# Kernel optimization log

Measured on AMD Instinct MI355X. Metric: run time of the kernel, lower is better.

## Reference

```python
import jax, jax.numpy as jnp
import numpy as np

N_NODES = 50000
N_EDGES = 800000
HIDDEN = 64


def _init_linear(key, fan_in, fan_out):
    kw, kb = jax.random.split(key)
    lim = 1.0 / np.sqrt(fan_in)
    W = jax.random.uniform(kw, (fan_in, fan_out), jnp.float32, -lim, lim)
    b = jax.random.uniform(kb, (fan_out,), jnp.float32, -lim, lim)
    return W, b


def setup_inputs() -> dict:
    key = jax.random.key(0)
    ks = jax.random.split(key, 10)
    feat = jax.random.normal(ks[0], (N_NODES, HIDDEN), jnp.float32)
    x = jax.random.normal(ks[1], (N_NODES, 3), jnp.float32)
    src = jax.random.randint(ks[2], (N_EDGES,), 0, N_NODES, jnp.int32)
    dst = jax.random.randint(ks[3], (N_EDGES,), 0, N_NODES, jnp.int32)
    # message MLP: (2H+1) -> H -> H, relu after both layers (last_activation=mid)
    W1, b1 = _init_linear(ks[4], 2 * HIDDEN + 1, HIDDEN)
    W2, b2 = _init_linear(ks[5], HIDDEN, HIDDEN)
    # soft edge gate: H -> 1
    we, be = _init_linear(ks[6], HIDDEN, 1)
    # update MLP: H -> H -> H, relu mid, no last activation
    U1, c1 = _init_linear(ks[7], HIDDEN, HIDDEN)
    U2, c2 = _init_linear(ks[8], HIDDEN, HIDDEN)
    return dict(feat=feat, x=x, src=src, dst=dst,
                W1=W1, b1=b1, W2=W2, b2=b2, we=we, be=be,
                U1=U1, c1=c1, U2=U2, c2=c2)


def reference(feat, x, src, dst, W1, b1, W2, b2, we, be, U1, c1, U2, c2):
    # per-edge squared distance between endpoint coordinates: [E, 1]
    sqd = jnp.sum((x[src] - x[dst]) ** 2, axis=-1, keepdims=True)
    # message input: [E, 2H+1]
    msg_in = jnp.concatenate([feat[src], feat[dst], sqd], axis=-1)
    # 2-layer message MLP with relu mid and last activation
    m = jax.nn.relu(jax.nn.relu(msg_in @ W1 + b1) @ W2 + b2)
    # sigmoid soft-edge gate: [E, 1]
    gate = jax.nn.sigmoid(m @ we + be)
    # scatter-sum gated messages to destination nodes: [N, H]
    m_sum = jax.ops.segment_sum(m * gate, dst, num_segments=N_NODES)
    # node update MLP on (m_sum + feat), residual add
    h = m_sum + feat
    h_new = jax.nn.relu(h @ U1 + c1) @ U2 + c2
    return h_new + feat
```

## Files before the change

kernel.cpp:

```cpp
#include <hip/hip_runtime.h>
#include <hip/hip_bf16.h>
#include <stdint.h>

#define N_NODES 50000
#define N_EDGES 800000
#define HDIM 64
#define SCAN_N (N_NODES + 1)

#define MSG_BYTES  ((size_t)N_EDGES * HDIM * 2)
#define INT_OFF    MSG_BYTES
#define DEG_OFF    (INT_OFF)
#define OFFS_OFF   (INT_OFF + 204800)
#define POS_OFF    (INT_OFF + 409600)
#define FB_OFF     (INT_OFF + 614400)
#define W1T_OFF    (FB_OFF + (size_t)N_NODES * HDIM * 2)
#define W2T_OFF    (W1T_OFF + 16384)
#define U1T_OFF    (W2T_OFF + 8192)
#define U2T_OFF    (U1T_OFF + 8192)
#define WS_NEED    (U2T_OFF + 8192)

typedef __attribute__((ext_vector_type(8))) short short8;
typedef __attribute__((ext_vector_type(4))) float floatx4;

__device__ __forceinline__ float bf2f(unsigned short u) {
    union { unsigned int i; float f; } v; v.i = ((unsigned int)u) << 16; return v.f;
}
__device__ __forceinline__ unsigned short f2bf(float f) {
    __hip_bfloat16 h = __float2bfloat16(f);
    return *reinterpret_cast<unsigned short*>(&h);
}

__device__ __forceinline__ int detect_is_bf16(const unsigned short* p) {
    int cnt = 0;
    #pragma unroll
    for (int i = 0; i < 64; ++i) {
        unsigned short b = p[i];
        int e = (b >> 7) & 0xFF;
        cnt += ((e >= 97 && e <= 157) || (b & 0x7FFF) == 0) ? 1 : 0;
    }
    return cnt >= 56;
}

__device__ __forceinline__ float getf(const void* p, unsigned int i, int isb) {
    return isb ? bf2f(((const unsigned short*)p)[i]) : ((const float*)p)[i];
}

__device__ __forceinline__ short8 get8bf(const void* p, unsigned int i, int isb) {
    if (isb) {
        return *reinterpret_cast<const short8*>((const short*)p + i);
    } else {
        const float4 f0 = *reinterpret_cast<const float4*>((const float*)p + i);
        const float4 f1 = *reinterpret_cast<const float4*>((const float*)p + i + 4);
        short8 a;
        a[0] = (short)f2bf(f0.x); a[1] = (short)f2bf(f0.y);
        a[2] = (short)f2bf(f0.z); a[3] = (short)f2bf(f0.w);
        a[4] = (short)f2bf(f1.x); a[5] = (short)f2bf(f1.y);
        a[6] = (short)f2bf(f1.z); a[7] = (short)f2bf(f1.w);
        return a;
    }
}

#define COMPILER_FENCE() asm volatile("" ::: "memory")
#define WAIT_LDS() __builtin_amdgcn_s_waitcnt(0xC07F)

__global__ __launch_bounds__(256) void cvt_kernel(const void* __restrict__ feat,
                                                  unsigned short* __restrict__ fb) {
    const int isb = detect_is_bf16((const unsigned short*)feat);
    int i = (blockIdx.x * 256 + threadIdx.x) * 8;
    if (i >= N_NODES * HDIM) return;
    if (isb) {
        *reinterpret_cast<uint4*>(fb + i) =
            *reinterpret_cast<const uint4*>((const unsigned short*)feat + i);
    } else {
        float4 f0 = *reinterpret_cast<const float4*>((const float*)feat + i);
        float4 f1 = *reinterpret_cast<const float4*>((const float*)feat + i + 4);
        ushort4 a = {f2bf(f0.x), f2bf(f0.y), f2bf(f0.z), f2bf(f0.w)};
        ushort4 b = {f2bf(f1.x), f2bf(f1.y), f2bf(f1.z), f2bf(f1.w)};
        *reinterpret_cast<ushort4*>(fb + i)     = a;
        *reinterpret_cast<ushort4*>(fb + i + 4) = b;
    }
}

__global__ __launch_bounds__(256) void prepw_kernel(
    const void* __restrict__ feat,
    const void* __restrict__ W1, const void* __restrict__ W2,
    const void* __restrict__ U1, const void* __restrict__ U2,
    unsigned short* __restrict__ w1t, unsigned short* __restrict__ w2t,
    unsigned short* __restrict__ u1t, unsigned short* __restrict__ u2t)
{
    const int isb = detect_is_bf16((const unsigned short*)feat);
    int idx = blockIdx.x * 256 + threadIdx.x;
    if (idx < 8192) {
        int n = idx >> 7, k = idx & 127;
        w1t[idx] = f2bf(getf(W1, k * 64 + n, isb));
    } else if (idx < 12288) {
        int i = idx - 8192, n = i >> 6, k = i & 63;
        w2t[i] = f2bf(getf(W2, k * 64 + n, isb));
    } else if (idx < 16384) {
        int i = idx - 12288, n = i >> 6, k = i & 63;
        u1t[i] = f2bf(getf(U1, k * 64 + n, isb));
    } else if (idx < 20480) {
        int i = idx - 16384, n = i >> 6, k = i & 63;
        u2t[i] = f2bf(getf(U2, k * 64 + n, isb));
    }
}

__global__ void hist_kernel(const int* __restrict__ dst, int* __restrict__ deg) {
    for (int e = blockIdx.x * blockDim.x + threadIdx.x; e < N_EDGES;
         e += gridDim.x * blockDim.x)
        atomicAdd(&deg[dst[e]], 1);
}

__global__ void scan1_kernel(const int* __restrict__ deg, int* __restrict__ part) {
    __shared__ int s[1024];
    int g = blockIdx.x * 1024 + threadIdx.x;
    s[threadIdx.x] = (g < SCAN_N) ? deg[g] : 0;
    __syncthreads();
    for (int off = 512; off > 0; off >>= 1) {
        if (threadIdx.x < off) s[threadIdx.x] += s[threadIdx.x + off];
        __syncthreads();
    }
    if (threadIdx.x == 0) part[blockIdx.x] = s[0];
}

__global__ void scan2_kernel(int* __restrict__ part, int nparts) {
    if (threadIdx.x == 0) {
        int run = 0;
        for (int i = 0; i < nparts; ++i) { int t = part[i]; part[i] = run; run += t; }
    }
}

__global__ void scan3_kernel(const int* __restrict__ deg, const int* __restrict__ part,
                             int* __restrict__ offs, int* __restrict__ pos) {
    __shared__ int s[1024];
    int g = blockIdx.x * 1024 + threadIdx.x;
    int v = (g < SCAN_N) ? deg[g] : 0;
    s[threadIdx.x] = v;
    __syncthreads();
    for (int off = 1; off < 1024; off <<= 1) {
        int t = (threadIdx.x >= off) ? s[threadIdx.x - off] : 0;
        __syncthreads();
        s[threadIdx.x] += t;
        __syncthreads();
    }
    int excl = s[threadIdx.x] - v + part[blockIdx.x];
    if (g < SCAN_N) { offs[g] = excl; pos[g] = excl; }
}

template <bool CSR>
__global__ __launch_bounds__(256, 2) void edge_kernel(
    const unsigned short* __restrict__ fbf,
    const unsigned short* __restrict__ w1t, const unsigned short* __restrict__ w2t,
    const void* __restrict__ feat, const void* __restrict__ xpos,
    const int* __restrict__ src, const int* __restrict__ dst,
    const void* __restrict__ W1, const void* __restrict__ b1,
    const void* __restrict__ W2, const void* __restrict__ b2,
    const void* __restrict__ we, const void* __restrict__ be,
    float* __restrict__ msum, unsigned int msum_cap,
    unsigned short* __restrict__ msg, int* __restrict__ pos)
{
    __shared__ __align__(16) short sA2[4][16][72];

    const int isb  = detect_is_bf16((const unsigned short*)feat);
    const int tid  = threadIdx.x;
    const int wave = tid >> 6;
    const int lane = tid & 63;
    const int l15  = lane & 15;
    const int quad = lane >> 4;

    short8 bw1[4][4];
    short8 bw2[2][4];
    if (CSR) {
        #pragma unroll
        for (int nt = 0; nt < 4; ++nt) {
            const int n = nt * 16 + l15;
            #pragma unroll
            for (int c = 0; c < 4; ++c)
                bw1[c][nt] = *reinterpret_cast<const short8*>(w1t + n * 128 + c * 32 + quad * 8);
            #pragma unroll
            for (int c = 0; c < 2; ++c)
                bw2[c][nt] = *reinterpret_cast<const short8*>(w2t + n * 64 + c * 32 + quad * 8);
        }
    } else {
        #pragma unroll
        for (int c = 0; c < 4; ++c)
            #pragma unroll
            for (int nt = 0; nt < 4; ++nt) {
                short8 b;
                #pragma unroll
                for (int j = 0; j < 8; ++j)
                    b[j] = (short)f2bf(getf(W1, (c * 32 + quad * 8 + j) * 64 + nt * 16 + l15, isb));
                bw1[c][nt] = b;
            }
        #pragma unroll
        for (int c = 0; c < 2; ++c)
            #pragma unroll
            for (int nt = 0; nt < 4; ++nt) {
                short8 b;
                #pragma unroll
                for (int j = 0; j < 8; ++j)
                    b[j] = (short)f2bf(getf(W2, (c * 32 + quad * 8 + j) * 64 + nt * 16 + l15, isb));
                bw2[c][nt] = b;
            }
    }
    float b1r[4], w1lr[4], b2r[4], wer[4];
    #pragma unroll
    for (int nt = 0; nt < 4; ++nt) {
        int n = nt * 16 + l15;
        b1r[nt]  = getf(b1, n, isb);
        w1lr[nt] = getf(W1, 128 * 64 + n, isb);
        b2r[nt]  = getf(b2, n, isb);
        wer[nt]  = getf(we, n, isb);
    }
    const float ber = getf(be, 0, isb);
    const int rowb = quad * 4;

    const int ntiles = N_EDGES / 64;
    for (int t = blockIdx.x; t < ntiles; t += gridDim.x) {
        const int ebase = t * 64 + wave * 16;

        int sidx = 0, didx = 0, slotv = 0;
        float sqd = 0.f;
        if (lane < 16) {
            int e = ebase + lane;
            sidx = src[e];
            didx = dst[e];
            if (CSR) slotv = atomicAdd(&pos[didx], 1);
            float dx = getf(xpos, sidx * 3 + 0, isb) - getf(xpos, didx * 3 + 0, isb);
            float dy = getf(xpos, sidx * 3 + 1, isb) - getf(xpos, didx * 3 + 1, isb);
            float dz = getf(xpos, sidx * 3 + 2, isb) - getf(xpos, didx * 3 + 2, isb);
            sqd = dx * dx + dy * dy + dz * dz;
        }
        const int sn     = __shfl(sidx, l15);
        const int dn_row = __shfl(didx, l15);

        floatx4 acc[4];
        #pragma unroll
        for (int nt = 0; nt < 4; ++nt) acc[nt] = (floatx4){0.f, 0.f, 0.f, 0.f};
        #pragma unroll
        for (int c = 0; c < 4; ++c) {
            const int node = (c < 2) ? sn : dn_row;
            const unsigned int aoff = (unsigned int)node * 64u + (c & 1) * 32 + quad * 8;
            short8 a;
            if (CSR) a = *reinterpret_cast<const short8*>((const short*)fbf + aoff);
            else     a = get8bf(feat, aoff, isb);
            #pragma unroll
            for (int nt = 0; nt < 4; ++nt)
                acc[nt] = __builtin_amdgcn_mfma_f32_16x16x32_bf16(a, bw1[c][nt], acc[nt], 0, 0, 0);
        }

        float sq[4];
        #pragma unroll
        for (int r = 0; r < 4; ++r) sq[r] = __shfl(sqd, rowb + r);
        #pragma unroll
        for (int nt = 0; nt < 4; ++nt)
            #pragma unroll
            for (int r = 0; r < 4; ++r) {
                float v = fmaxf(acc[nt][r] + b1r[nt] + sq[r] * w1lr[nt], 0.f);
                sA2[wave][rowb + r][nt * 16 + l15] = (short)f2bf(v);
            }
        COMPILER_FENCE();
        WAIT_LDS();

        floatx4 acc2[4];
        #pragma unroll
        for (int nt = 0; nt < 4; ++nt) acc2[nt] = (floatx4){0.f, 0.f, 0.f, 0.f};
        #pragma unroll
        for (int c = 0; c < 2; ++c) {
            short8 a = *reinterpret_cast<const short8*>(&sA2[wave][l15][c * 32 + quad * 8]);
            #pragma unroll
            for (int nt = 0; nt < 4; ++nt)
                acc2[nt] = __builtin_amdgcn_mfma_f32_16x16x32_bf16(a, bw2[c][nt], acc2[nt], 0, 0, 0);
        }
        COMPILER_FENCE();

        float mval[4][4];
        float part[4] = {0.f, 0.f, 0.f, 0.f};
        #pragma unroll
        for (int nt = 0; nt < 4; ++nt)
            #pragma unroll
            for (int r = 0; r < 4; ++r) {
                float v = fmaxf(acc2[nt][r] + b2r[nt], 0.f);
                mval[nt][r] = v;
                part[r] += v * wer[nt];
            }
        #pragma unroll
        for (int off = 1; off < 16; off <<= 1)
            #pragma unroll
            for (int r = 0; r < 4; ++r) part[r] += __shfl_xor(part[r], off);
        float gate[4];
        #pragma unroll
        for (int r = 0; r < 4; ++r)
            gate[r] = 1.f / (1.f + __expf(-(part[r] + ber)));

        if (CSR) {
            #pragma unroll
            for (int nt = 0; nt < 4; ++nt)
                #pragma unroll
                for (int r = 0; r < 4; ++r)
                    sA2[wave][rowb + r][nt * 16 + l15] = (short)f2bf(mval[nt][r] * gate[r]);
            COMPILER_FENCE();
            WAIT_LDS();
            int slot_r = __shfl(slotv, l15);
            const short8 v0 = *reinterpret_cast<const short8*>(&sA2[wave][l15][quad * 16]);
            const short8 v1 = *reinterpret_cast<const short8*>(&sA2[wave][l15][quad * 16 + 8]);
            unsigned short* mp = msg + (size_t)slot_r * 64 + quad * 16;
            *reinterpret_cast<short8*>(mp)     = v0;
            *reinterpret_cast<short8*>(mp + 8) = v1;
            COMPILER_FENCE();
        } else {
            #pragma unroll
            for (int r = 0; r < 4; ++r) {
                int dn = __shfl(didx, rowb + r);
                unsigned int base = (unsigned int)dn * 64u;
                if (base + 64u <= msum_cap) {
                    #pragma unroll
                    for (int nt = 0; nt < 4; ++nt)
                        unsafeAtomicAdd(&msum[base + nt * 16 + l15], mval[nt][r] * gate[r]);
                }
            }
        }
    }
}

template <bool MSGRED>
__global__ __launch_bounds__(256, 2) void node_kernel(
    const unsigned short* __restrict__ msg, const int* __restrict__ offs,
    const float* __restrict__ msum,
    const unsigned short* __restrict__ u1t, const unsigned short* __restrict__ u2t,
    const void* __restrict__ feat,
    const void* __restrict__ U1, const void* __restrict__ c1v,
    const void* __restrict__ U2, const void* __restrict__ c2v,
    void* __restrict__ out)
{
    __shared__ __align__(16) short sT[4][16][72];
    __shared__ __align__(16) float sF[4][16][68];

    const int isb  = detect_is_bf16((const unsigned short*)feat);
    const int tid  = threadIdx.x;
    const int wave = tid >> 6;
    const int lane = tid & 63;
    const int l15  = lane & 15;
    const int quad = lane >> 4;

    short8 u1f[2][4], u2f[2][4];
    if (MSGRED) {
        #pragma unroll
        for (int nt = 0; nt < 4; ++nt) {
            const int n = nt * 16 + l15;
            #pragma unroll
            for (int c = 0; c < 2; ++c) {
                u1f[c][nt] = *reinterpret_cast<const short8*>(u1t + n * 64 + c * 32 + quad * 8);
                u2f[c][nt] = *reinterpret_cast<const short8*>(u2t + n * 64 + c * 32 + quad * 8);
            }
        }
    } else {
        #pragma unroll
        for (int c = 0; c < 2; ++c)
            #pragma unroll
            for (int nt = 0; nt < 4; ++nt) {
                short8 a, b;
                #pragma unroll
                for (int j = 0; j < 8; ++j) {
                    int k = c * 32 + quad * 8 + j, n = nt * 16 + l15;
                    a[j] = (short)f2bf(getf(U1, k * 64 + n, isb));
                    b[j] = (short)f2bf(getf(U2, k * 64 + n, isb));
                }
                u1f[c][nt] = a; u2f[c][nt] = b;
            }
    }
    float c1r[4], c2r[4];
    #pragma unroll
    for (int nt = 0; nt < 4; ++nt) {
        c1r[nt] = getf(c1v, nt * 16 + l15, isb);
        c2r[nt] = getf(c2v, nt * 16 + l15, isb);
    }
    const int rowb = quad * 4;

    const int ntile = (N_NODES + 15) / 16;
    const int t = blockIdx.x * 4 + wave;
    if (t < ntile) {
        const int node = t * 16 + l15;

        float acc16[16];
        #pragma unroll
        for (int i = 0; i < 16; ++i) acc16[i] = 0.f;
        if (MSGRED) {
            int s = offs[node], e = offs[node + 1];
            for (int j = s; j < e; ++j) {
                const unsigned short* p = msg + (size_t)j * 64 + quad * 8;
                short8 a0 = *reinterpret_cast<const short8*>(p);
                short8 a1 = *reinterpret_cast<const short8*>(p + 32);
                #pragma unroll
                for (int i = 0; i < 8; ++i) {
                    acc16[i]     += bf2f((unsigned short)a0[i]);
                    acc16[8 + i] += bf2f((unsigned short)a1[i]);
                }
            }
        } else {
            #pragma unroll
            for (int c = 0; c < 2; ++c) {
                unsigned int off = (unsigned int)node * 64u + c * 32 + quad * 8;
                float4 m0 = *reinterpret_cast<const float4*>(msum + off);
                float4 m1 = *reinterpret_cast<const float4*>(msum + off + 4);
                acc16[c * 8 + 0] = m0.x; acc16[c * 8 + 1] = m0.y;
                acc16[c * 8 + 2] = m0.z; acc16[c * 8 + 3] = m0.w;
                acc16[c * 8 + 4] = m1.x; acc16[c * 8 + 5] = m1.y;
                acc16[c * 8 + 6] = m1.z; acc16[c * 8 + 7] = m1.w;
            }
        }

        short8 ah[2];
        #pragma unroll
        for (int c = 0; c < 2; ++c) {
            unsigned int off = (unsigned int)node * 64u + c * 32 + quad * 8;
            float hv[8];
            if (isb) {
                short8 fv = *reinterpret_cast<const short8*>((const short*)feat + off);
                #pragma unroll
                for (int j = 0; j < 8; ++j) hv[j] = bf2f((unsigned short)fv[j]);
            } else {
                float4 f0 = *reinterpret_cast<const float4*>((const float*)feat + off);
                float4 f1 = *reinterpret_cast<const float4*>((const float*)feat + off + 4);
                hv[0] = f0.x; hv[1] = f0.y; hv[2] = f0.z; hv[3] = f0.w;
                hv[4] = f1.x; hv[5] = f1.y; hv[6] = f1.z; hv[7] = f1.w;
            }
            short8 a;
            #pragma unroll
            for (int j = 0; j < 8; ++j) a[j] = (short)f2bf(acc16[c * 8 + j] + hv[j]);
            ah[c] = a;
        }

        floatx4 acc[4];
        #pragma unroll
        for (int nt = 0; nt < 4; ++nt) acc[nt] = (floatx4){0.f, 0.f, 0.f, 0.f};
        #pragma unroll
        for (int c = 0; c < 2; ++c)
            #pragma unroll
            for (int nt = 0; nt < 4; ++nt)
                acc[nt] = __builtin_amdgcn_mfma_f32_16x16x32_bf16(ah[c], u1f[c][nt], acc[nt], 0, 0, 0);

        #pragma unroll
        for (int nt = 0; nt < 4; ++nt)
            #pragma unroll
            for (int r = 0; r < 4; ++r) {
                float v = fmaxf(acc[nt][r] + c1r[nt], 0.f);
                sT[wave][rowb + r][nt * 16 + l15] = (short)f2bf(v);
            }
        COMPILER_FENCE();
        WAIT_LDS();

        floatx4 acc2[4];
        #pragma unroll
        for (int nt = 0; nt < 4; ++nt) acc2[nt] = (floatx4){0.f, 0.f, 0.f, 0.f};
        #pragma unroll
        for (int c = 0; c < 2; ++c) {
            short8 a = *reinterpret_cast<const short8*>(&sT[wave][l15][c * 32 + quad * 8]);
            #pragma unroll
            for (int nt = 0; nt < 4; ++nt)
                acc2[nt] = __builtin_amdgcn_mfma_f32_16x16x32_bf16(a, u2f[c][nt], acc2[nt], 0, 0, 0);
        }
        COMPILER_FENCE();

        #pragma unroll
        for (int nt = 0; nt < 4; ++nt)
            #pragma unroll
            for (int r = 0; r < 4; ++r)
                sF[wave][rowb + r][nt * 16 + l15] = acc2[nt][r] + c2r[nt];
        COMPILER_FENCE();
        WAIT_LDS();

        const unsigned int ob = (unsigned int)node * 64u + quad * 16;
        if (isb) {
            const unsigned short* fp = (const unsigned short*)feat + ob;
            unsigned short* op = (unsigned short*)out + ob;
            #pragma unroll
            for (int k = 0; k < 2; ++k) {
                ushort4 o0, o1;
                float4 v0 = *reinterpret_cast<const float4*>(&sF[wave][l15][quad * 16 + k * 8]);
                float4 v1 = *reinterpret_cast<const float4*>(&sF[wave][l15][quad * 16 + k * 8 + 4]);
                const ushort4 f0 = *reinterpret_cast<const ushort4*>(fp + k * 8);
                const ushort4 f1 = *reinterpret_cast<const ushort4*>(fp + k * 8 + 4);
                o0.x = f2bf(v0.x + bf2f(f0.x)); o0.y = f2bf(v0.y + bf2f(f0.y));
                o0.z = f2bf(v0.z + bf2f(f0.z)); o0.w = f2bf(v0.w + bf2f(f0.w));
                o1.x = f2bf(v1.x + bf2f(f1.x)); o1.y = f2bf(v1.y + bf2f(f1.y));
                o1.z = f2bf(v1.z + bf2f(f1.z)); o1.w = f2bf(v1.w + bf2f(f1.w));
                *reinterpret_cast<ushort4*>(op + k * 8)     = o0;
                *reinterpret_cast<ushort4*>(op + k * 8 + 4) = o1;
            }
        } else {
            const float* fp = (const float*)feat + ob;
            float* op = (float*)out + ob;
            #pragma unroll
            for (int k = 0; k < 4; ++k) {
                float4 v = *reinterpret_cast<const float4*>(&sF[wave][l15][quad * 16 + k * 4]);
                float4 f = *reinterpret_cast<const float4*>(fp + k * 4);
                float4 o = {v.x + f.x, v.y + f.y, v.z + f.z, v.w + f.w};
                *reinterpret_cast<float4*>(op + k * 4) = o;
            }
        }
        COMPILER_FENCE();
    }
}

extern "C" void kernel_launch(void* const* d_in, const int* in_sizes, int n_in,
                              void* d_out, int out_size, void* d_ws, size_t ws_size,
                              hipStream_t stream) {
    const void* feat = d_in[0];
    const void* x    = d_in[1];
    const int* src   = (const int*)d_in[2];
    const int* dst   = (const int*)d_in[3];
    const void* W1   = d_in[4];
    const void* b1   = d_in[5];
    const void* W2   = d_in[6];
    const void* b2   = d_in[7];
    const void* we   = d_in[8];
    const void* be   = d_in[9];
    const void* U1   = d_in[10];
    const void* c1   = d_in[11];
    const void* U2   = d_in[12];
    const void* c2   = d_in[13];
    char* ws = (char*)d_ws;

    if (ws_size >= WS_NEED) {
        unsigned short* msg = (unsigned short*)(ws);
        int* deg  = (int*)(ws + DEG_OFF);
        int* offs = (int*)(ws + OFFS_OFF);
        int* pos  = (int*)(ws + POS_OFF);
        unsigned short* fb  = (unsigned short*)(ws + FB_OFF);
        unsigned short* w1t = (unsigned short*)(ws + W1T_OFF);
        unsigned short* w2t = (unsigned short*)(ws + W2T_OFF);
        unsigned short* u1t = (unsigned short*)(ws + U1T_OFF);
        unsigned short* u2t = (unsigned short*)(ws + U2T_OFF);

        hipMemsetAsync(deg, 0, 204800, stream);
        cvt_kernel<<<(N_NODES * HDIM / 8 + 255) / 256, 256, 0, stream>>>(feat, fb);
        prepw_kernel<<<80, 256, 0, stream>>>(feat, W1, W2, U1, U2, w1t, w2t, u1t, u2t);
        hist_kernel<<<1024, 256, 0, stream>>>(dst, deg);
        scan1_kernel<<<49, 1024, 0, stream>>>(deg, offs + 51200 - 64);
        scan2_kernel<<<1, 64, 0, stream>>>(offs + 51200 - 64, 49);
        scan3_kernel<<<49, 1024, 0, stream>>>(deg, offs + 51200 - 64, offs, pos);
        edge_kernel<true><<<2500, 256, 0, stream>>>(fb, w1t, w2t, feat, x, src, dst,
                                                    W1, b1, W2, b2, we, be,
                                                    nullptr, 0xFFFFFFFFu, msg, pos);
        node_kernel<true><<<((N_NODES + 15) / 16 + 3) / 4, 256, 0, stream>>>(
            msg, offs, nullptr, u1t, u2t, feat, U1, c1, U2, c2, d_out);
    } else {
        float* msum = (float*)ws;
        size_t need = (size_t)N_NODES * HDIM * sizeof(float);
        size_t clr  = need < ws_size ? need : ws_size;
        unsigned int cap = (unsigned int)(ws_size / sizeof(float));
        if (cap > (unsigned int)(N_NODES * HDIM)) cap = (unsigned int)(N_NODES * HDIM);

        hipMemsetAsync(msum, 0, clr, stream);
        edge_kernel<false><<<2500, 256, 0, stream>>>(nullptr, nullptr, nullptr, feat, x, src, dst,
                                                     W1, b1, W2, b2, we, be,
                                                     msum, cap, nullptr, nullptr);
        node_kernel<false><<<((N_NODES + 15) / 16 + 3) / 4, 256, 0, stream>>>(
            nullptr, nullptr, msum, nullptr, nullptr, feat, U1, c1, U2, c2, d_out);
    }
}
```

Before: 278.0 us.

## Fuse prep kernels, stage MLP weights in LDS, unroll CSR message reduction

Merges the feature-convert, weight-transpose and degree-histogram kernels into one launch split by block index, removing two launches. The edge kernel now keeps W1/W2 fragments in shared memory instead of 24 short8 registers per lane, which frees registers for occupancy but adds LDS reads inside the MFMA loop. The node kernel's CSR reduction processes two messages per iteration with a second accumulator set to expose more memory-level parallelism.

```diff
diff --git a/kernel.cpp b/kernel.cpp
--- a/kernel.cpp
+++ b/kernel.cpp
@@ -18,6 +18,10 @@
 #define U1T_OFF    (W2T_OFF + 8192)
 #define U2T_OFF    (U1T_OFF + 8192)
 #define WS_NEED    (U2T_OFF + 8192)
+
+#define CVT_BLOCKS  1563
+#define PREPW_BLOCKS 80
+#define HIST_BLOCKS 1024
 
 typedef __attribute__((ext_vector_type(8))) short short8;
 typedef __attribute__((ext_vector_type(4))) float floatx4;
@@ -63,52 +67,51 @@
 #define COMPILER_FENCE() asm volatile("" ::: "memory")
 #define WAIT_LDS() __builtin_amdgcn_s_waitcnt(0xC07F)
 
-__global__ __launch_bounds__(256) void cvt_kernel(const void* __restrict__ feat,
-                                                  unsigned short* __restrict__ fb) {
-    const int isb = detect_is_bf16((const unsigned short*)feat);
-    int i = (blockIdx.x * 256 + threadIdx.x) * 8;
-    if (i >= N_NODES * HDIM) return;
-    if (isb) {
-        *reinterpret_cast<uint4*>(fb + i) =
-            *reinterpret_cast<const uint4*>((const unsigned short*)feat + i);
-    } else {
-        float4 f0 = *reinterpret_cast<const float4*>((const float*)feat + i);
-        float4 f1 = *reinterpret_cast<const float4*>((const float*)feat + i + 4);
-        ushort4 a = {f2bf(f0.x), f2bf(f0.y), f2bf(f0.z), f2bf(f0.w)};
-        ushort4 b = {f2bf(f1.x), f2bf(f1.y), f2bf(f1.z), f2bf(f1.w)};
-        *reinterpret_cast<ushort4*>(fb + i)     = a;
-        *reinterpret_cast<ushort4*>(fb + i + 4) = b;
-    }
-}
-
-__global__ __launch_bounds__(256) void prepw_kernel(
-    const void* __restrict__ feat,
+__global__ __launch_bounds__(256) void prep_kernel(
+    const void* __restrict__ feat, unsigned short* __restrict__ fb,
     const void* __restrict__ W1, const void* __restrict__ W2,
     const void* __restrict__ U1, const void* __restrict__ U2,
     unsigned short* __restrict__ w1t, unsigned short* __restrict__ w2t,
-    unsigned short* __restrict__ u1t, unsigned short* __restrict__ u2t)
+    unsigned short* __restrict__ u1t, unsigned short* __restrict__ u2t,
+    const int* __restrict__ dst, int* __restrict__ deg)
 {
-    const int isb = detect_is_bf16((const unsigned short*)feat);
-    int idx = blockIdx.x * 256 + threadIdx.x;
-    if (idx < 8192) {
-        int n = idx >> 7, k = idx & 127;
-        w1t[idx] = f2bf(getf(W1, k * 64 + n, isb));
-    } else if (idx < 12288) {
-        int i = idx - 8192, n = i >> 6, k = i & 63;
-        w2t[i] = f2bf(getf(W2, k * 64 + n, isb));
-    } else if (idx < 16384) {
-        int i = idx - 12288, n = i >> 6, k = i & 63;
-        u1t[i] = f2bf(getf(U1, k * 64 + n, isb));
-    } else if (idx < 20480) {
-        int i = idx - 16384, n = i >> 6, k = i & 63;
-        u2t[i] = f2bf(getf(U2, k * 64 + n, isb));
-    }
-}
-
-__global__ void hist_kernel(const int* __restrict__ dst, int* __restrict__ deg) {
-    for (int e = blockIdx.x * blockDim.x + threadIdx.x; e < N_EDGES;
-         e += gridDim.x * blockDim.x)
-        atomicAdd(&deg[dst[e]], 1);
+    const int b = blockIdx.x;
+    if (b < CVT_BLOCKS) {
+        const int isb = detect_is_bf16((const unsigned short*)feat);
+        int i = (b * 256 + threadIdx.x) * 8;
+        if (i >= N_NODES * HDIM) return;
+        if (isb) {
+            *reinterpret_cast<uint4*>(fb + i) =
+                *reinterpret_cast<const uint4*>((const unsigned short*)feat + i);
+        } else {
+            float4 f0 = *reinterpret_cast<const float4*>((const float*)feat + i);
+            float4 f1 = *reinterpret_cast<const float4*>((const float*)feat + i + 4);
+            ushort4 a = {f2bf(f0.x), f2bf(f0.y), f2bf(f0.z), f2bf(f0.w)};
+            ushort4 c = {f2bf(f1.x), f2bf(f1.y), f2bf(f1.z), f2bf(f1.w)};
+            *reinterpret_cast<ushort4*>(fb + i)     = a;
+            *reinterpret_cast<ushort4*>(fb + i + 4) = c;
+        }
+    } else if (b < CVT_BLOCKS + PREPW_BLOCKS) {
+        const int isb = detect_is_bf16((const unsigned short*)feat);
+        int idx = (b - CVT_BLOCKS) * 256 + threadIdx.x;
+        if (idx < 8192) {
+            int n = idx >> 7, k = idx & 127;
+            w1t[idx] = f2bf(getf(W1, k * 64 + n, isb));
+        } else if (idx < 12288) {
+            int i = idx - 8192, n = i >> 6, k = i & 63;
+            w2t[i] = f2bf(getf(W2, k * 64 + n, isb));
+        } else if (idx < 16384) {
+            int i = idx - 12288, n = i >> 6, k = i & 63;
+            u1t[i] = f2bf(getf(U1, k * 64 + n, isb));
+        } else if (idx < 20480) {
+            int i = idx - 16384, n = i >> 6, k = i & 63;
+            u2t[i] = f2bf(getf(U2, k * 64 + n, isb));
+        }
+    } else {
+        int e0 = (b - CVT_BLOCKS - PREPW_BLOCKS) * 256 + threadIdx.x;
+        for (int e = e0; e < N_EDGES; e += HIST_BLOCKS * 256)
+            atomicAdd(&deg[dst[e]], 1);
+    }
 }
 
 __global__ void scan1_kernel(const int* __restrict__ deg, int* __restrict__ part) {
@@ -159,6 +162,8 @@
     float* __restrict__ msum, unsigned int msum_cap,
     unsigned short* __restrict__ msg, int* __restrict__ pos)
 {
+    __shared__ __align__(16) short sW1[16][64][8];
+    __shared__ __align__(16) short sW2[8][64][8];
     __shared__ __align__(16) short sA2[4][16][72];
 
     const int isb  = detect_is_bf16((const unsigned short*)feat);
@@ -171,16 +176,21 @@
     short8 bw1[4][4];
     short8 bw2[2][4];
     if (CSR) {
-        #pragma unroll
-        for (int nt = 0; nt < 4; ++nt) {
-            const int n = nt * 16 + l15;
-            #pragma unroll
-            for (int c = 0; c < 4; ++c)
-                bw1[c][nt] = *reinterpret_cast<const short8*>(w1t + n * 128 + c * 32 + quad * 8);
-            #pragma unroll
-            for (int c = 0; c < 2; ++c)
-                bw2[c][nt] = *reinterpret_cast<const short8*>(w2t + n * 64 + c * 32 + quad * 8);
-        }
+        for (int i = tid; i < 16 * 64; i += 256) {
+            int f = i >> 6, l = i & 63;
+            int n = (f & 3) * 16 + (l & 15);
+            int k0 = (f >> 2) * 32 + (l >> 4) * 8;
+            *reinterpret_cast<short8*>(&sW1[f][l][0]) =
+                *reinterpret_cast<const short8*>(w1t + n * 128 + k0);
+        }
+        for (int i = tid; i < 8 * 64; i += 256) {
+            int f = i >> 6, l = i & 63;
+            int n = (f & 3) * 16 + (l & 15);
+            int k0 = (f >> 2) * 32 + (l >> 4) * 8;
+            *reinterpret_cast<short8*>(&sW2[f][l][0]) =
+                *reinterpret_cast<const short8*>(w2t + n * 64 + k0);
+        }
+        __syncthreads();
     } else {
         #pragma unroll
         for (int c = 0; c < 4; ++c)
@@ -203,6 +213,7 @@
                 bw2[c][nt] = b;
             }
     }
+
     float b1r[4], w1lr[4], b2r[4], wer[4];
     #pragma unroll
     for (int nt = 0; nt < 4; ++nt) {
@@ -245,8 +256,12 @@
             if (CSR) a = *reinterpret_cast<const short8*>((const short*)fbf + aoff);
             else     a = get8bf(feat, aoff, isb);
             #pragma unroll
-            for (int nt = 0; nt < 4; ++nt)
-                acc[nt] = __builtin_amdgcn_mfma_f32_16x16x32_bf16(a, bw1[c][nt], acc[nt], 0, 0, 0);
+            for (int nt = 0; nt < 4; ++nt) {
+                short8 b;
+                if (CSR) b = *reinterpret_cast<const short8*>(&sW1[c * 4 + nt][lane][0]);
+                else     b = bw1[c][nt];
+                acc[nt] = __builtin_amdgcn_mfma_f32_16x16x32_bf16(a, b, acc[nt], 0, 0, 0);
+            }
         }
 
         float sq[4];
@@ -269,8 +284,12 @@
         for (int c = 0; c < 2; ++c) {
             short8 a = *reinterpret_cast<const short8*>(&sA2[wave][l15][c * 32 + quad * 8]);
             #pragma unroll
-            for (int nt = 0; nt < 4; ++nt)
-                acc2[nt] = __builtin_amdgcn_mfma_f32_16x16x32_bf16(a, bw2[c][nt], acc2[nt], 0, 0, 0);
+            for (int nt = 0; nt < 4; ++nt) {
+                short8 b;
+                if (CSR) b = *reinterpret_cast<const short8*>(&sW2[c * 4 + nt][lane][0]);
+                else     b = bw2[c][nt];
+                acc2[nt] = __builtin_amdgcn_mfma_f32_16x16x32_bf16(a, b, acc2[nt], 0, 0, 0);
+            }
         }
         COMPILER_FENCE();
 
@@ -386,17 +405,38 @@
         #pragma unroll
         for (int i = 0; i < 16; ++i) acc16[i] = 0.f;
         if (MSGRED) {
+            float accB[16];
+            #pragma unroll
+            for (int i = 0; i < 16; ++i) accB[i] = 0.f;
             int s = offs[node], e = offs[node + 1];
-            for (int j = s; j < e; ++j) {
-                const unsigned short* p = msg + (size_t)j * 64 + quad * 8;
-                short8 a0 = *reinterpret_cast<const short8*>(p);
-                short8 a1 = *reinterpret_cast<const short8*>(p + 32);
+            int j = s;
+            for (; j + 1 < e; j += 2) {
+                const unsigned short* p0 = msg + (size_t)j * 64 + quad * 8;
+                const unsigned short* p1 = msg + (size_t)(j + 1) * 64 + quad * 8;
+                short8 a0 = *reinterpret_cast<const short8*>(p0);
+                short8 a1 = *reinterpret_cast<const short8*>(p0 + 32);
+                short8 b0 = *reinterpret_cast<const short8*>(p1);
+                short8 b1 = *reinterpret_cast<const short8*>(p1 + 32);
+                #pragma unroll
+                for (int i = 0; i < 8; ++i) {
+                    acc16[i]     += bf2f((unsigned short)a0[i]);
+                    acc16[8 + i] += bf2f((unsigned short)a1[i]);
+                    accB[i]      += bf2f((unsigned short)b0[i]);
+                    accB[8 + i]  += bf2f((unsigned short)b1[i]);
+                }
+            }
+            if (j < e) {
+                const unsigned short* p0 = msg + (size_t)j * 64 + quad * 8;
+                short8 a0 = *reinterpret_cast<const short8*>(p0);
+                short8 a1 = *reinterpret_cast<const short8*>(p0 + 32);
                 #pragma unroll
                 for (int i = 0; i < 8; ++i) {
                     acc16[i]     += bf2f((unsigned short)a0[i]);
                     acc16[8 + i] += bf2f((unsigned short)a1[i]);
                 }
             }
+            #pragma unroll
+            for (int i = 0; i < 16; ++i) acc16[i] += accB[i];
         } else {
             #pragma unroll
             for (int c = 0; c < 2; ++c) {
@@ -534,9 +574,8 @@
         unsigned short* u2t = (unsigned short*)(ws + U2T_OFF);
 
         hipMemsetAsync(deg, 0, 204800, stream);
-        cvt_kernel<<<(N_NODES * HDIM / 8 + 255) / 256, 256, 0, stream>>>(feat, fb);
-        prepw_kernel<<<80, 256, 0, stream>>>(feat, W1, W2, U1, U2, w1t, w2t, u1t, u2t);
-        hist_kernel<<<1024, 256, 0, stream>>>(dst, deg);
+        prep_kernel<<<CVT_BLOCKS + PREPW_BLOCKS + HIST_BLOCKS, 256, 0, stream>>>(
+            feat, fb, W1, W2, U1, U2, w1t, w2t, u1t, u2t, dst, deg);
         scan1_kernel<<<49, 1024, 0, stream>>>(deg, offs + 51200 - 64);
         scan2_kernel<<<1, 64, 0, stream>>>(offs + 51200 - 64, 49);
         scan3_kernel<<<49, 1024, 0, stream>>>(deg, offs + 51200 - 64, offs, pos);
```

After: 251.1 us. 1.11x faster.
